# Optimization experiments

Measured on AMD Instinct MI355X. Metric: run time of the kernel, lower is better.

## Reference

```python
import jax, jax.numpy as jnp
import numpy as np

N_USER = 50000
N_ITEM = 100000
N = N_USER + N_ITEM
D = 64
NNZ = 2_400_000
B = 4096
N_LAYERS = 3
NEG_SLOPE = 0.01  # F.leaky_relu default
EPS = 1e-12       # F.normalize default eps


def setup_inputs() -> dict:
    key = jax.random.key(0)
    ks = jax.random.split(key, 12)
    s = 0.1  # xavier-ish scale
    return {
        "user_emb": jax.random.normal(ks[0], (N_USER, D), jnp.float32) * s,
        "item_emb": jax.random.normal(ks[1], (N_ITEM, D), jnp.float32) * s,
        "W_gc": jax.random.normal(ks[2], (N_LAYERS, D, D), jnp.float32) * s,
        "W_bi": jax.random.normal(ks[3], (N_LAYERS, D, D), jnp.float32) * s,
        "b_bi": jax.random.normal(ks[4], (N_LAYERS, 1, D), jnp.float32) * s,
        "vals": jax.random.uniform(ks[5], (NNZ,), jnp.float32) * (1.0 / 16.0),
        "rows": jax.random.randint(ks[6], (NNZ,), 0, N, jnp.int32),
        "cols": jax.random.randint(ks[7], (NNZ,), 0, N, jnp.int32),
        "users": jax.random.randint(ks[8], (B,), 0, N_USER, jnp.int32),
        "pos_items": jax.random.randint(ks[9], (B,), 0, N_ITEM, jnp.int32),
        "neg_items": jax.random.randint(ks[10], (B,), 0, N_ITEM, jnp.int32),
    }


def _spmm(rows, cols, vals, E, n):
    # sparse [n,n] (COO) @ dense [n,d]
    return jax.ops.segment_sum(vals[:, None] * E[cols], rows, num_segments=n)


def reference(user_emb, item_emb, W_gc, W_bi, b_bi, vals, rows, cols,
              users, pos_items, neg_items):
    n_user = user_emb.shape[0]
    n = n_user + item_emb.shape[0]
    ego = jnp.concatenate([user_emb, item_emb], axis=0)  # [N, D]
    all_embs = [ego]
    for k in range(N_LAYERS):
        L_side = _spmm(rows, cols, vals, ego, n)        # L @ E
        LI_side = L_side + ego                           # (L + I) @ E
        # NOTE: original code adds b_bi to BOTH branches (b_gc unused)
        sum_e = LI_side @ W_gc[k] + b_bi[k]
        bi_e = (L_side * ego) @ W_bi[k] + b_bi[k]
        ego = jax.nn.leaky_relu(sum_e + bi_e, NEG_SLOPE)
        norm = ego / jnp.maximum(
            jnp.linalg.norm(ego, axis=1, keepdims=True), EPS)
        all_embs.append(norm)
    all_embs = jnp.concatenate(all_embs, axis=1)         # [N, D*(L+1)]
    u_g = all_embs[:n_user][users]
    pos_g = all_embs[n_user:][pos_items]
    neg_g = all_embs[n_user:][neg_items]
    return (u_g, pos_g, neg_g)
```

## Files before the change

### kernel.cpp

```cpp
#include <hip/hip_runtime.h>

#define N_USER 50000
#define N_ITEM 100000
#define NTOT   150000
#define D      64
#define NNZ    2400000
#define NEG_SLOPE 0.01f

#define BSHIFT 10
#define NB     147
#define P1_PER 4096
#define NBLK1  586
#define NROWBLK 2344

typedef unsigned int uint;
typedef unsigned short ushort;
typedef _Float16 h4 __attribute__((ext_vector_type(4)));
typedef float f4 __attribute__((ext_vector_type(4)));

__device__ inline uint bf16rne(float x) {
    uint b = __float_as_uint(x);
    return (b + 0x7FFFu + ((b >> 16) & 1u)) >> 16;
}
__device__ inline float bf_lo(uint u) { return __uint_as_float(u << 16); }
__device__ inline float bf_hi(uint u) { return __uint_as_float(u & 0xFFFF0000u); }

__global__ void k_concat16(const float* __restrict__ u, const float* __restrict__ it,
                           ushort* __restrict__ A16) {
    int i = blockIdx.x * 256 + threadIdx.x;
    const int nu4 = N_USER * D / 4;
    float4 v = (i < nu4) ? ((const float4*)u)[i] : ((const float4*)it)[i - nu4];
    uint lo = bf16rne(v.x) | (bf16rne(v.y) << 16);
    uint hi = bf16rne(v.z) | (bf16rne(v.w) << 16);
    ((uint2*)A16)[i] = make_uint2(lo, hi);
}

__global__ void k_bzero(int* __restrict__ bcnt) {
    int t = threadIdx.x;
    if (t < NB) bcnt[t] = 0;
}

__global__ __launch_bounds__(1024) void k_bhist(const int* __restrict__ rows,
                                                int* __restrict__ bcnt) {
    __shared__ int lcnt[NB];
    int tid = threadIdx.x;
    if (tid < NB) lcnt[tid] = 0;
    __syncthreads();
    int base = blockIdx.x * P1_PER;
    #pragma unroll
    for (int k = 0; k < 4; ++k) {
        int i = base + k * 1024 + tid;
        if (i < NNZ) atomicAdd(&lcnt[rows[i] >> BSHIFT], 1);
    }
    __syncthreads();
    if (tid < NB) atomicAdd(&bcnt[tid], lcnt[tid]);
}

__global__ void k_bscan(const int* __restrict__ bcnt, int* __restrict__ bptr,
                        int* __restrict__ bcur) {
    __shared__ int s[256];
    int tid = threadIdx.x;
    int v = (tid < NB) ? bcnt[tid] : 0;
    s[tid] = v; __syncthreads();
    for (int off = 1; off < 256; off <<= 1) {
        int t = (tid >= off) ? s[tid - off] : 0;
        __syncthreads();
        s[tid] += t;
        __syncthreads();
    }
    if (tid < NB) { int ex = s[tid] - v; bptr[tid] = ex; bcur[tid] = ex; }
    if (tid == NB - 1) bptr[NB] = s[tid];
}

__global__ __launch_bounds__(1024) void k_binpass1(const int* __restrict__ rows,
                                                   const int* __restrict__ cols,
                                                   const float* __restrict__ vals,
                                                   int* __restrict__ bcur,
                                                   int2* __restrict__ bucketed) {
    __shared__ int lcnt[NB], lbase[NB];
    int tid = threadIdx.x;
    int base = blockIdx.x * P1_PER;
    if (tid < NB) lcnt[tid] = 0;
    __syncthreads();
    int r[4];
    #pragma unroll
    for (int k = 0; k < 4; ++k) {
        int i = base + k * 1024 + tid;
        r[k] = (i < NNZ) ? rows[i] : -1;
        if (r[k] >= 0) atomicAdd(&lcnt[r[k] >> BSHIFT], 1);
    }
    __syncthreads();
    if (tid < NB) { lbase[tid] = atomicAdd(&bcur[tid], lcnt[tid]); lcnt[tid] = 0; }
    __syncthreads();
    #pragma unroll
    for (int k = 0; k < 4; ++k) {
        int i = base + k * 1024 + tid;
        if (r[k] >= 0) {
            int b = r[k] >> BSHIFT;
            int off = atomicAdd(&lcnt[b], 1);
            bucketed[lbase[b] + off] =
                make_int2(((r[k] & 1023) << 18) | cols[i], __float_as_int(vals[i]));
        }
    }
}

__global__ __launch_bounds__(1024) void k_binpass2(const int* __restrict__ bptr,
                                                   const int2* __restrict__ bucketed,
                                                   int* __restrict__ ptr,
                                                   int2* __restrict__ csr) {
    __shared__ int c0[1024], px[1024];
    int tid = threadIdx.x, b = blockIdx.x;
    int s = bptr[b], e = bptr[b + 1];
    c0[tid] = 0;
    __syncthreads();
    for (int i = s + tid; i < e; i += 1024) atomicAdd(&c0[bucketed[i].x >> 18], 1);
    __syncthreads();
    int v = c0[tid];
    px[tid] = v;
    __syncthreads();
    for (int off = 1; off < 1024; off <<= 1) {
        int t = (tid >= off) ? px[tid - off] : 0;
        __syncthreads();
        px[tid] += t;
        __syncthreads();
    }
    int ex = px[tid] - v;
    int r = (b << BSHIFT) + tid;
    if (r <= NTOT) ptr[r] = s + ex;
    px[tid] = ex;
    c0[tid] = 0;
    __syncthreads();
    for (int i = s + tid; i < e; i += 1024) {
        int2 e2 = bucketed[i];
        int lr = e2.x >> 18;
        int off = atomicAdd(&c0[lr], 1);
        csr[s + px[lr] + off] = make_int2(e2.x & 0x3FFFF, e2.y);
    }
}

__global__ __launch_bounds__(256) void k_spmm(const int* __restrict__ ptr,
                                              const int2* __restrict__ csr,
                                              const ushort* __restrict__ E16,
                                              float* __restrict__ Lout) {
    int lane = threadIdx.x & 63;
    int half = lane >> 5;
    int l32  = lane & 31;
    int r = __builtin_amdgcn_readfirstlane(blockIdx.x * 4 + (threadIdx.x >> 6));
    int start = ptr[r], end = ptr[r + 1];
    float acc0 = 0.f, acc1 = 0.f;
    const uint* E32 = (const uint*)E16;
    int j = start;
    for (; j + 15 < end; j += 16) {
        int2 ea0 = csr[j + 0],  ea1 = csr[j + 1],  ea2 = csr[j + 2],  ea3 = csr[j + 3];
        int2 ea4 = csr[j + 4],  ea5 = csr[j + 5],  ea6 = csr[j + 6],  ea7 = csr[j + 7];
        int2 ea8 = csr[j + 8],  ea9 = csr[j + 9],  eaA = csr[j + 10], eaB = csr[j + 11];
        int2 eaC = csr[j + 12], eaD = csr[j + 13], eaE = csr[j + 14], eaF = csr[j + 15];
        int c0 = half ? ea1.x : ea0.x;
        int c1 = half ? ea3.x : ea2.x;
        int c2 = half ? ea5.x : ea4.x;
        int c3 = half ? ea7.x : ea6.x;
        int c4 = half ? ea9.x : ea8.x;
        int c5 = half ? eaB.x : eaA.x;
        int c6 = half ? eaD.x : eaC.x;
        int c7 = half ? eaF.x : eaE.x;
        uint u0 = E32[(c0 << 5) + l32];
        uint u1 = E32[(c1 << 5) + l32];
        uint u2 = E32[(c2 << 5) + l32];
        uint u3 = E32[(c3 << 5) + l32];
        uint u4 = E32[(c4 << 5) + l32];
        uint u5 = E32[(c5 << 5) + l32];
        uint u6 = E32[(c6 << 5) + l32];
        uint u7 = E32[(c7 << 5) + l32];
        float v0 = __int_as_float(half ? ea1.y : ea0.y);
        float v1 = __int_as_float(half ? ea3.y : ea2.y);
        float v2 = __int_as_float(half ? ea5.y : ea4.y);
        float v3 = __int_as_float(half ? ea7.y : ea6.y);
        float v4 = __int_as_float(half ? ea9.y : ea8.y);
        float v5 = __int_as_float(half ? eaB.y : eaA.y);
        float v6 = __int_as_float(half ? eaD.y : eaC.y);
        float v7 = __int_as_float(half ? eaF.y : eaE.y);
        acc0 += v0 * bf_lo(u0);  acc1 += v0 * bf_hi(u0);
        acc0 += v1 * bf_lo(u1);  acc1 += v1 * bf_hi(u1);
        acc0 += v2 * bf_lo(u2);  acc1 += v2 * bf_hi(u2);
        acc0 += v3 * bf_lo(u3);  acc1 += v3 * bf_hi(u3);
        acc0 += v4 * bf_lo(u4);  acc1 += v4 * bf_hi(u4);
        acc0 += v5 * bf_lo(u5);  acc1 += v5 * bf_hi(u5);
        acc0 += v6 * bf_lo(u6);  acc1 += v6 * bf_hi(u6);
        acc0 += v7 * bf_lo(u7);  acc1 += v7 * bf_hi(u7);
    }
    for (; j + 7 < end; j += 8) {
        int2 ea = csr[j + 0], eb = csr[j + 1];
        int2 ec = csr[j + 2], ed = csr[j + 3];
        int2 ee = csr[j + 4], ef = csr[j + 5];
        int2 eg = csr[j + 6], eh = csr[j + 7];
        int c0 = half ? eb.x : ea.x;
        int c1 = half ? ed.x : ec.x;
        int c2 = half ? ef.x : ee.x;
        int c3 = half ? eh.x : eg.x;
        uint u0 = E32[(c0 << 5) + l32];
        uint u1 = E32[(c1 << 5) + l32];
        uint u2 = E32[(c2 << 5) + l32];
        uint u3 = E32[(c3 << 5) + l32];
        float v0 = __int_as_float(half ? eb.y : ea.y);
        float v1 = __int_as_float(half ? ed.y : ec.y);
        float v2 = __int_as_float(half ? ef.y : ee.y);
        float v3 = __int_as_float(half ? eh.y : eg.y);
        acc0 += v0 * bf_lo(u0);  acc1 += v0 * bf_hi(u0);
        acc0 += v1 * bf_lo(u1);  acc1 += v1 * bf_hi(u1);
        acc0 += v2 * bf_lo(u2);  acc1 += v2 * bf_hi(u2);
        acc0 += v3 * bf_lo(u3);  acc1 += v3 * bf_hi(u3);
    }
    for (; j + 1 < end; j += 2) {
        int2 ea = csr[j], eb = csr[j + 1];
        int c   = half ? eb.x : ea.x;
        float v = __int_as_float(half ? eb.y : ea.y);
        uint u = E32[(c << 5) + l32];
        acc0 += v * bf_lo(u);  acc1 += v * bf_hi(u);
    }
    if (j < end) {
        int2 ea = csr[j];
        if (half == 0) {
            uint u = E32[(ea.x << 5) + l32];
            float v = __int_as_float(ea.y);
            acc0 += v * bf_lo(u);  acc1 += v * bf_hi(u);
        }
    }
    acc0 += __shfl_xor(acc0, 32, 64);
    acc1 += __shfl_xor(acc1, 32, 64);
    if (half == 0)
        *(float2*)&Lout[r * D + l32 * 2] = make_float2(acc0, acc1);
}

__global__ __launch_bounds__(256) void k_transform_mfma(
        const ushort* __restrict__ E16, const float* __restrict__ L,
        const float* __restrict__ Wgc, const float* __restrict__ Wbi,
        const float* __restrict__ bb, ushort* __restrict__ O16, int n) {
    __shared__ _Float16 ldsW[2 * 16 * 256];
    __shared__ ushort   ldsO[4][16 * 72];
    int tid = threadIdx.x;

    #pragma unroll
    for (int m = 0; m < 2; ++m) {
        const float* W = m ? Wbi : Wgc;
        for (int idx = tid; idx < 4096; idx += 256) {
            int k = idx >> 6, nn = idx & 63;
            ldsW[(m * 16 + (k >> 4) * 4 + (nn >> 4)) * 256 + (nn & 15) * 16 + (k & 15)] =
                (_Float16)W[idx];
        }
    }
    __syncthreads();

    int l = tid & 63, w = tid >> 6;
    int g = l >> 4, r16 = l & 15;

    h4 bfrag[2][4][4];
    #pragma unroll
    for (int m = 0; m < 2; ++m)
        #pragma unroll
        for (int ks = 0; ks < 4; ++ks)
            #pragma unroll
            for (int nt = 0; nt < 4; ++nt)
                bfrag[m][ks][nt] =
                    *(const h4*)&ldsW[(m * 16 + ks * 4 + nt) * 256 + r16 * 16 + g * 4];

    int rowbase = blockIdx.x * 64 + w * 16;
    int r = rowbase + r16;
    int rc = min(r, n - 1);

    h4 x1[4], x2[4];
    #pragma unroll
    for (int ks = 0; ks < 4; ++ks) {
        int c = ks * 16 + g * 4;
        float4 lf = *(const float4*)&L[rc * D + c];
        uint2  eu = *(const uint2*)&E16[rc * D + c];
        float e0 = bf_lo(eu.x), e1 = bf_hi(eu.x);
        float e2 = bf_lo(eu.y), e3 = bf_hi(eu.y);
        x1[ks][0] = (_Float16)(lf.x + e0); x1[ks][1] = (_Float16)(lf.y + e1);
        x1[ks][2] = (_Float16)(lf.z + e2); x1[ks][3] = (_Float16)(lf.w + e3);
        x2[ks][0] = (_Float16)(lf.x * e0); x2[ks][1] = (_Float16)(lf.y * e1);
        x2[ks][2] = (_Float16)(lf.z * e2); x2[ks][3] = (_Float16)(lf.w * e3);
    }

    f4 acc[4];
    #pragma unroll
    for (int nt = 0; nt < 4; ++nt) acc[nt] = (f4){0.f, 0.f, 0.f, 0.f};
    #pragma unroll
    for (int ks = 0; ks < 4; ++ks)
        #pragma unroll
        for (int nt = 0; nt < 4; ++nt)
            acc[nt] = __builtin_amdgcn_mfma_f32_16x16x16f16(x1[ks], bfrag[0][ks][nt],
                                                            acc[nt], 0, 0, 0);
    #pragma unroll
    for (int ks = 0; ks < 4; ++ks)
        #pragma unroll
        for (int nt = 0; nt < 4; ++nt)
            acc[nt] = __builtin_amdgcn_mfma_f32_16x16x16f16(x2[ks], bfrag[1][ks][nt],
                                                            acc[nt], 0, 0, 0);

    #pragma unroll
    for (int nt = 0; nt < 4; ++nt) {
        int col = nt * 16 + r16;
        float bv = 2.f * bb[col];
        #pragma unroll
        for (int i = 0; i < 4; ++i) {
            float y = acc[nt][i] + bv;
            y = (y >= 0.f) ? y : NEG_SLOPE * y;
            ldsO[w][(g * 4 + i) * 72 + col] = (ushort)bf16rne(y);
        }
    }
    int lr = l >> 2;
    int rowg = rowbase + lr;
    if (rowg < n) {
        const ushort* src = &ldsO[w][lr * 72 + (l & 3) * 16];
        uint4 v0 = *(const uint4*)src;
        uint4 v1 = *(const uint4*)(src + 8);
        *(uint4*)&O16[rowg * D + (l & 3) * 16] = v0;
        *(uint4*)&O16[rowg * D + (l & 3) * 16 + 8] = v1;
    }
}

__global__ void k_gather0(const float* __restrict__ u, const float* __restrict__ it,
                          const int* __restrict__ users, const int* __restrict__ pos,
                          const int* __restrict__ neg, float* __restrict__ out) {
    int lane = threadIdx.x & 63;
    int gi = blockIdx.x * 4 + (threadIdx.x >> 6);
    int g = gi >> 12, b = gi & 4095;
    const float* src = (g == 0) ? (u + (size_t)users[b] * D)
                                : (it + (size_t)((g == 1) ? pos[b] : neg[b]) * D);
    out[gi * 256 + lane] = src[lane];
}

__global__ void k_gathern(const ushort* __restrict__ E16, const int* __restrict__ users,
                          const int* __restrict__ pos, const int* __restrict__ neg,
                          float* __restrict__ out, int layer) {
    int lane = threadIdx.x & 63;
    int gi = blockIdx.x * 4 + (threadIdx.x >> 6);
    int g = gi >> 12, b = gi & 4095;
    int src = (g == 0) ? users[b] : (N_USER + ((g == 1) ? pos[b] : neg[b]));
    float v = __uint_as_float(((uint)E16[src * D + lane]) << 16);
    float ss = v * v;
    #pragma unroll
    for (int off = 32; off >= 1; off >>= 1) ss += __shfl_xor(ss, off, 64);
    float dnm = fmaxf(sqrtf(ss), 1e-12f);
    out[gi * 256 + layer * D + lane] = v / dnm;
}

extern "C" void kernel_launch(void* const* d_in, const int* in_sizes, int n_in,
                              void* d_out, int out_size, void* d_ws, size_t ws_size,
                              hipStream_t stream) {
    const float* user_emb = (const float*)d_in[0];
    const float* item_emb = (const float*)d_in[1];
    const float* W_gc     = (const float*)d_in[2];
    const float* W_bi     = (const float*)d_in[3];
    const float* b_bi     = (const float*)d_in[4];
    const float* vals     = (const float*)d_in[5];
    const int*   rows     = (const int*)d_in[6];
    const int*   cols     = (const int*)d_in[7];
    const int*   users    = (const int*)d_in[8];
    const int*   pos      = (const int*)d_in[9];
    const int*   neg      = (const int*)d_in[10];
    float* out = (float*)d_out;

    char* ws = (char*)d_ws;
    size_t off = 0;
    auto alloc = [&](size_t b) { void* p = ws + off; off += (b + 255) & ~(size_t)255; return p; };
    ushort* Ea  = (ushort*)alloc((size_t)NTOT * D * 2);
    ushort* Eb  = (ushort*)alloc((size_t)NTOT * D * 2);
    float*  L   = (float*) alloc((size_t)NTOT * D * 4);
    int2*   csr = (int2*)  alloc((size_t)NNZ * 8);
    int*    ptr = (int*)   alloc((size_t)(NTOT + 64) * 4);
    int*    bptr= (int*)   alloc((NB + 1) * 4);
    int*    bcnt= (int*)   alloc(NB * 4);
    int*    bcur= (int*)   alloc(NB * 4);
    int2*   bucketed = (int2*)L;
    (void)ws_size;

    hipLaunchKernelGGL(k_concat16, dim3(9375), dim3(256),  0, stream, user_emb, item_emb, Ea);
    hipLaunchKernelGGL(k_bzero,    dim3(1),    dim3(256),  0, stream, bcnt);
    hipLaunchKernelGGL(k_bhist,    dim3(NBLK1),dim3(1024), 0, stream, rows, bcnt);
    hipLaunchKernelGGL(k_bscan,    dim3(1),    dim3(256),  0, stream, bcnt, bptr, bcur);
    hipLaunchKernelGGL(k_binpass1, dim3(NBLK1),dim3(1024), 0, stream, rows, cols, vals, bcur, bucketed);
    hipLaunchKernelGGL(k_binpass2, dim3(NB),   dim3(1024), 0, stream, bptr, bucketed, ptr, csr);
    hipLaunchKernelGGL(k_gather0,  dim3(3072), dim3(256),  0, stream, user_emb, item_emb, users, pos, neg, out);

    ushort* cur = Ea; ushort* nxt = Eb;
    for (int k = 0; k < 3; ++k) {
        hipLaunchKernelGGL(k_spmm,           dim3(37500),  dim3(256), 0, stream, ptr, csr, cur, L);
        hipLaunchKernelGGL(k_transform_mfma, dim3(NROWBLK),dim3(256), 0, stream, cur, L,
                           W_gc + k * 4096, W_bi + k * 4096, b_bi + k * 64, nxt, NTOT);
        hipLaunchKernelGGL(k_gathern,        dim3(3072),   dim3(256), 0, stream, nxt, users, pos, neg, out, k + 1);
        ushort* t = cur; cur = nxt; nxt = t;
    }
}
```

Before: 453.0 us.

## Switch embeddings and L buffer to fp16 and fuse small setup kernels

Stores the embedding tables and the SpMM output L in fp16 instead of bf16 embeddings plus an fp32 L. This halves the write and read traffic of L between the spmm and transform kernels and removes the element-wise fp16 conversions of the transform inputs. The bucket-count zeroing moves into the concat kernel and the scan merges with the layer-0 gather, cutting two launches. The bucketed buffer gets its own allocation instead of aliasing L. fp16 has less range than bf16 and rounds L a second time, though values here are small.

Result: no change. 450.3 us (-0.6%).

```diff
diff --git a/kernel.cpp b/kernel.cpp
--- a/kernel.cpp
+++ b/kernel.cpp
@@ -15,29 +15,20 @@
 
 typedef unsigned int uint;
 typedef unsigned short ushort;
+typedef _Float16 h2 __attribute__((ext_vector_type(2)));
 typedef _Float16 h4 __attribute__((ext_vector_type(4)));
 typedef float f4 __attribute__((ext_vector_type(4)));
 
-__device__ inline uint bf16rne(float x) {
-    uint b = __float_as_uint(x);
-    return (b + 0x7FFFu + ((b >> 16) & 1u)) >> 16;
-}
-__device__ inline float bf_lo(uint u) { return __uint_as_float(u << 16); }
-__device__ inline float bf_hi(uint u) { return __uint_as_float(u & 0xFFFF0000u); }
-
 __global__ void k_concat16(const float* __restrict__ u, const float* __restrict__ it,
-                           ushort* __restrict__ A16) {
+                           ushort* __restrict__ A16, int* __restrict__ bcnt) {
+    if (blockIdx.x == 0 && threadIdx.x < NB) bcnt[threadIdx.x] = 0;
     int i = blockIdx.x * 256 + threadIdx.x;
     const int nu4 = N_USER * D / 4;
     float4 v = (i < nu4) ? ((const float4*)u)[i] : ((const float4*)it)[i - nu4];
-    uint lo = bf16rne(v.x) | (bf16rne(v.y) << 16);
-    uint hi = bf16rne(v.z) | (bf16rne(v.w) << 16);
-    ((uint2*)A16)[i] = make_uint2(lo, hi);
-}
-
-__global__ void k_bzero(int* __restrict__ bcnt) {
-    int t = threadIdx.x;
-    if (t < NB) bcnt[t] = 0;
+    h2 a, b;
+    a.x = (_Float16)v.x; a.y = (_Float16)v.y;
+    b.x = (_Float16)v.z; b.y = (_Float16)v.w;
+    ((uint2*)A16)[i] = make_uint2(__builtin_bit_cast(uint, a), __builtin_bit_cast(uint, b));
 }
 
 __global__ __launch_bounds__(1024) void k_bhist(const int* __restrict__ rows,
@@ -56,20 +47,32 @@
     if (tid < NB) atomicAdd(&bcnt[tid], lcnt[tid]);
 }
 
-__global__ void k_bscan(const int* __restrict__ bcnt, int* __restrict__ bptr,
-                        int* __restrict__ bcur) {
+__global__ void k_bscan_gather(const int* __restrict__ bcnt, int* __restrict__ bptr,
+                               int* __restrict__ bcur,
+                               const float* __restrict__ u, const float* __restrict__ it,
+                               const int* __restrict__ users, const int* __restrict__ pos,
+                               const int* __restrict__ neg, float* __restrict__ out) {
     __shared__ int s[256];
-    int tid = threadIdx.x;
-    int v = (tid < NB) ? bcnt[tid] : 0;
-    s[tid] = v; __syncthreads();
-    for (int off = 1; off < 256; off <<= 1) {
-        int t = (tid >= off) ? s[tid - off] : 0;
-        __syncthreads();
-        s[tid] += t;
-        __syncthreads();
-    }
-    if (tid < NB) { int ex = s[tid] - v; bptr[tid] = ex; bcur[tid] = ex; }
-    if (tid == NB - 1) bptr[NB] = s[tid];
+    if (blockIdx.x == 3072) {
+        int tid = threadIdx.x;
+        int v = (tid < NB) ? bcnt[tid] : 0;
+        s[tid] = v; __syncthreads();
+        for (int off = 1; off < 256; off <<= 1) {
+            int t = (tid >= off) ? s[tid - off] : 0;
+            __syncthreads();
+            s[tid] += t;
+            __syncthreads();
+        }
+        if (tid < NB) { int ex = s[tid] - v; bptr[tid] = ex; bcur[tid] = ex; }
+        if (tid == NB - 1) bptr[NB] = s[tid];
+        return;
+    }
+    int lane = threadIdx.x & 63;
+    int gi = blockIdx.x * 4 + (threadIdx.x >> 6);
+    int g = gi >> 12, b = gi & 4095;
+    const float* src = (g == 0) ? (u + (size_t)users[b] * D)
+                                : (it + (size_t)((g == 1) ? pos[b] : neg[b]) * D);
+    out[gi * 256 + lane] = src[lane];
 }
 
 __global__ __launch_bounds__(1024) void k_binpass1(const int* __restrict__ rows,
@@ -141,7 +144,7 @@
 __global__ __launch_bounds__(256) void k_spmm(const int* __restrict__ ptr,
                                               const int2* __restrict__ csr,
                                               const ushort* __restrict__ E16,
-                                              float* __restrict__ Lout) {
+                                              ushort* __restrict__ L16) {
     int lane = threadIdx.x & 63;
     int half = lane >> 5;
     int l32  = lane & 31;
@@ -179,14 +182,18 @@
         float v5 = __int_as_float(half ? eaB.y : eaA.y);
         float v6 = __int_as_float(half ? eaD.y : eaC.y);
         float v7 = __int_as_float(half ? eaF.y : eaE.y);
-        acc0 += v0 * bf_lo(u0);  acc1 += v0 * bf_hi(u0);
-        acc0 += v1 * bf_lo(u1);  acc1 += v1 * bf_hi(u1);
-        acc0 += v2 * bf_lo(u2);  acc1 += v2 * bf_hi(u2);
-        acc0 += v3 * bf_lo(u3);  acc1 += v3 * bf_hi(u3);
-        acc0 += v4 * bf_lo(u4);  acc1 += v4 * bf_hi(u4);
-        acc0 += v5 * bf_lo(u5);  acc1 += v5 * bf_hi(u5);
-        acc0 += v6 * bf_lo(u6);  acc1 += v6 * bf_hi(u6);
-        acc0 += v7 * bf_lo(u7);  acc1 += v7 * bf_hi(u7);
+        h2 p0 = __builtin_bit_cast(h2, u0), p1 = __builtin_bit_cast(h2, u1);
+        h2 p2 = __builtin_bit_cast(h2, u2), p3 = __builtin_bit_cast(h2, u3);
+        h2 p4 = __builtin_bit_cast(h2, u4), p5 = __builtin_bit_cast(h2, u5);
+        h2 p6 = __builtin_bit_cast(h2, u6), p7 = __builtin_bit_cast(h2, u7);
+        acc0 += v0 * (float)p0.x;  acc1 += v0 * (float)p0.y;
+        acc0 += v1 * (float)p1.x;  acc1 += v1 * (float)p1.y;
+        acc0 += v2 * (float)p2.x;  acc1 += v2 * (float)p2.y;
+        acc0 += v3 * (float)p3.x;  acc1 += v3 * (float)p3.y;
+        acc0 += v4 * (float)p4.x;  acc1 += v4 * (float)p4.y;
+        acc0 += v5 * (float)p5.x;  acc1 += v5 * (float)p5.y;
+        acc0 += v6 * (float)p6.x;  acc1 += v6 * (float)p6.y;
+        acc0 += v7 * (float)p7.x;  acc1 += v7 * (float)p7.y;
     }
     for (; j + 7 < end; j += 8) {
         int2 ea = csr[j + 0], eb = csr[j + 1];
@@ -205,34 +212,38 @@
         float v1 = __int_as_float(half ? ed.y : ec.y);
         float v2 = __int_as_float(half ? ef.y : ee.y);
         float v3 = __int_as_float(half ? eh.y : eg.y);
-        acc0 += v0 * bf_lo(u0);  acc1 += v0 * bf_hi(u0);
-        acc0 += v1 * bf_lo(u1);  acc1 += v1 * bf_hi(u1);
-        acc0 += v2 * bf_lo(u2);  acc1 += v2 * bf_hi(u2);
-        acc0 += v3 * bf_lo(u3);  acc1 += v3 * bf_hi(u3);
+        h2 p0 = __builtin_bit_cast(h2, u0), p1 = __builtin_bit_cast(h2, u1);
+        h2 p2 = __builtin_bit_cast(h2, u2), p3 = __builtin_bit_cast(h2, u3);
+        acc0 += v0 * (float)p0.x;  acc1 += v0 * (float)p0.y;
+        acc0 += v1 * (float)p1.x;  acc1 += v1 * (float)p1.y;
+        acc0 += v2 * (float)p2.x;  acc1 += v2 * (float)p2.y;
+        acc0 += v3 * (float)p3.x;  acc1 += v3 * (float)p3.y;
     }
     for (; j + 1 < end; j += 2) {
         int2 ea = csr[j], eb = csr[j + 1];
         int c   = half ? eb.x : ea.x;
         float v = __int_as_float(half ? eb.y : ea.y);
-        uint u = E32[(c << 5) + l32];
-        acc0 += v * bf_lo(u);  acc1 += v * bf_hi(u);
+        h2 p = __builtin_bit_cast(h2, E32[(c << 5) + l32]);
+        acc0 += v * (float)p.x;  acc1 += v * (float)p.y;
     }
     if (j < end) {
         int2 ea = csr[j];
         if (half == 0) {
-            uint u = E32[(ea.x << 5) + l32];
+            h2 p = __builtin_bit_cast(h2, E32[(ea.x << 5) + l32]);
             float v = __int_as_float(ea.y);
-            acc0 += v * bf_lo(u);  acc1 += v * bf_hi(u);
+            acc0 += v * (float)p.x;  acc1 += v * (float)p.y;
         }
     }
     acc0 += __shfl_xor(acc0, 32, 64);
     acc1 += __shfl_xor(acc1, 32, 64);
-    if (half == 0)
-        *(float2*)&Lout[r * D + l32 * 2] = make_float2(acc0, acc1);
+    if (half == 0) {
+        h2 o; o.x = (_Float16)acc0; o.y = (_Float16)acc1;
+        ((uint*)L16)[(r << 5) + l32] = __builtin_bit_cast(uint, o);
+    }
 }
 
 __global__ __launch_bounds__(256) void k_transform_mfma(
-        const ushort* __restrict__ E16, const float* __restrict__ L,
+        const ushort* __restrict__ E16, const ushort* __restrict__ L16,
         const float* __restrict__ Wgc, const float* __restrict__ Wbi,
         const float* __restrict__ bb, ushort* __restrict__ O16, int n) {
     __shared__ _Float16 ldsW[2 * 16 * 256];
@@ -270,15 +281,16 @@
     h4 x1[4], x2[4];
     #pragma unroll
     for (int ks = 0; ks < 4; ++ks) {
-        int c = ks * 16 + g * 4;
-        float4 lf = *(const float4*)&L[rc * D + c];
-        uint2  eu = *(const uint2*)&E16[rc * D + c];
-        float e0 = bf_lo(eu.x), e1 = bf_hi(eu.x);
-        float e2 = bf_lo(eu.y), e3 = bf_hi(eu.y);
-        x1[ks][0] = (_Float16)(lf.x + e0); x1[ks][1] = (_Float16)(lf.y + e1);
-        x1[ks][2] = (_Float16)(lf.z + e2); x1[ks][3] = (_Float16)(lf.w + e3);
-        x2[ks][0] = (_Float16)(lf.x * e0); x2[ks][1] = (_Float16)(lf.y * e1);
-        x2[ks][2] = (_Float16)(lf.z * e2); x2[ks][3] = (_Float16)(lf.w * e3);
+        int ui = (rc << 5) + ks * 8 + g * 2;
+        uint2 lw = *(const uint2*)&((const uint*)L16)[ui];
+        uint2 ew = *(const uint2*)&((const uint*)E16)[ui];
+        h4 l4, e4;
+        h2 la = __builtin_bit_cast(h2, lw.x), lb = __builtin_bit_cast(h2, lw.y);
+        h2 ea = __builtin_bit_cast(h2, ew.x), eb = __builtin_bit_cast(h2, ew.y);
+        l4[0] = la.x; l4[1] = la.y; l4[2] = lb.x; l4[3] = lb.y;
+        e4[0] = ea.x; e4[1] = ea.y; e4[2] = eb.x; e4[3] = eb.y;
+        x1[ks] = l4 + e4;
+        x2[ks] = l4 * e4;
     }
 
     f4 acc[4];
@@ -305,7 +317,7 @@
         for (int i = 0; i < 4; ++i) {
             float y = acc[nt][i] + bv;
             y = (y >= 0.f) ? y : NEG_SLOPE * y;
-            ldsO[w][(g * 4 + i) * 72 + col] = (ushort)bf16rne(y);
+            ldsO[w][(g * 4 + i) * 72 + col] = __builtin_bit_cast(ushort, (_Float16)y);
         }
     }
     int lr = l >> 2;
@@ -319,17 +331,6 @@
     }
 }
 
-__global__ void k_gather0(const float* __restrict__ u, const float* __restrict__ it,
-                          const int* __restrict__ users, const int* __restrict__ pos,
-                          const int* __restrict__ neg, float* __restrict__ out) {
-    int lane = threadIdx.x & 63;
-    int gi = blockIdx.x * 4 + (threadIdx.x >> 6);
-    int g = gi >> 12, b = gi & 4095;
-    const float* src = (g == 0) ? (u + (size_t)users[b] * D)
-                                : (it + (size_t)((g == 1) ? pos[b] : neg[b]) * D);
-    out[gi * 256 + lane] = src[lane];
-}
-
 __global__ void k_gathern(const ushort* __restrict__ E16, const int* __restrict__ users,
                           const int* __restrict__ pos, const int* __restrict__ neg,
                           float* __restrict__ out, int layer) {
@@ -337,7 +338,7 @@
     int gi = blockIdx.x * 4 + (threadIdx.x >> 6);
     int g = gi >> 12, b = gi & 4095;
     int src = (g == 0) ? users[b] : (N_USER + ((g == 1) ? pos[b] : neg[b]));
-    float v = __uint_as_float(((uint)E16[src * D + lane]) << 16);
+    float v = (float)__builtin_bit_cast(_Float16, E16[src * D + lane]);
     float ss = v * v;
     #pragma unroll
     for (int off = 32; off >= 1; off >>= 1) ss += __shfl_xor(ss, off, 64);
@@ -366,27 +367,26 @@
     auto alloc = [&](size_t b) { void* p = ws + off; off += (b + 255) & ~(size_t)255; return p; };
     ushort* Ea  = (ushort*)alloc((size_t)NTOT * D * 2);
     ushort* Eb  = (ushort*)alloc((size_t)NTOT * D * 2);
-    float*  L   = (float*) alloc((size_t)NTOT * D * 4);
+    ushort* L16 = (ushort*)alloc((size_t)NTOT * D * 2);
     int2*   csr = (int2*)  alloc((size_t)NNZ * 8);
     int*    ptr = (int*)   alloc((size_t)(NTOT + 64) * 4);
     int*    bptr= (int*)   alloc((NB + 1) * 4);
     int*    bcnt= (int*)   alloc(NB * 4);
     int*    bcur= (int*)   alloc(NB * 4);
-    int2*   bucketed = (int2*)L;
+    int2*   bucketed = (int2*)alloc((size_t)NNZ * 8);
     (void)ws_size;
 
-    hipLaunchKernelGGL(k_concat16, dim3(9375), dim3(256),  0, stream, user_emb, item_emb, Ea);
-    hipLaunchKernelGGL(k_bzero,    dim3(1),    dim3(256),  0, stream, bcnt);
-    hipLaunchKernelGGL(k_bhist,    dim3(NBLK1),dim3(1024), 0, stream, rows, bcnt);
-    hipLaunchKernelGGL(k_bscan,    dim3(1),    dim3(256),  0, stream, bcnt, bptr, bcur);
-    hipLaunchKernelGGL(k_binpass1, dim3(NBLK1),dim3(1024), 0, stream, rows, cols, vals, bcur, bucketed);
-    hipLaunchKernelGGL(k_binpass2, dim3(NB),   dim3(1024), 0, stream, bptr, bucketed, ptr, csr);
-    hipLaunchKernelGGL(k_gather0,  dim3(3072), dim3(256),  0, stream, user_emb, item_emb, users, pos, neg, out);
+    hipLaunchKernelGGL(k_concat16,    dim3(9375), dim3(256),  0, stream, user_emb, item_emb, Ea, bcnt);
+    hipLaunchKernelGGL(k_bhist,       dim3(NBLK1),dim3(1024), 0, stream, rows, bcnt);
+    hipLaunchKernelGGL(k_bscan_gather,dim3(3073), dim3(256),  0, stream, bcnt, bptr, bcur,
+                       user_emb, item_emb, users, pos, neg, out);
+    hipLaunchKernelGGL(k_binpass1,    dim3(NBLK1),dim3(1024), 0, stream, rows, cols, vals, bcur, bucketed);
+    hipLaunchKernelGGL(k_binpass2,    dim3(NB),   dim3(1024), 0, stream, bptr, bucketed, ptr, csr);
 
     ushort* cur = Ea; ushort* nxt = Eb;
     for (int k = 0; k < 3; ++k) {
-        hipLaunchKernelGGL(k_spmm,           dim3(37500),  dim3(256), 0, stream, ptr, csr, cur, L);
-        hipLaunchKernelGGL(k_transform_mfma, dim3(NROWBLK),dim3(256), 0, stream, cur, L,
+        hipLaunchKernelGGL(k_spmm,           dim3(37500),  dim3(256), 0, stream, ptr, csr, cur, L16);
+        hipLaunchKernelGGL(k_transform_mfma, dim3(NROWBLK),dim3(256), 0, stream, cur, L16,
                            W_gc + k * 4096, W_bi + k * 4096, b_bi + k * 64, nxt, NTOT);
         hipLaunchKernelGGL(k_gathern,        dim3(3072),   dim3(256), 0, stream, nxt, users, pos, neg, out, k + 1);
         ushort* t = cur; cur = nxt; nxt = t;
```
